# Optimization experiments

Hardware: AMD Instinct MI355X
Metric: run time of the kernel (lower is better)

## Reference

```python
import jax, jax.numpy as jnp
import numpy as np

B, N, E = 256, 4096, 65536  # graphs, nodes/graph (64*64), edges/graph


def setup_inputs() -> dict:
    key = jax.random.key(0)
    k = jax.random.split(key, 6)
    x = jax.random.normal(k[0], (B, N, 3), dtype=jnp.float32)
    src = jax.random.randint(k[1], (E,), 0, N, dtype=jnp.int32)
    dst = jax.random.randint(k[2], (E,), 0, N, dtype=jnp.int32)
    W1 = jax.random.normal(k[3], (3, 64), dtype=jnp.float32) * 0.3
    b1 = jnp.zeros((64,), dtype=jnp.float32)
    Wfc = jax.random.normal(k[4], (N * 64, 1), dtype=jnp.float32) * 0.002
    bfc = jnp.zeros((1,), dtype=jnp.float32)
    return {"x": x, "W1": W1, "b1": b1, "Wfc": Wfc, "bfc": bfc,
            "src": src, "dst": dst}


def reference(x, W1, b1, Wfc, bfc, src, dst):
    # DGL GraphConv, norm='both': h = relu(D_in^{-1/2} A D_out^{-1/2} x W + b)
    ones = jnp.ones((E,), dtype=x.dtype)
    deg_out = jax.ops.segment_sum(ones, src, num_segments=N)
    deg_in = jax.ops.segment_sum(ones, dst, num_segments=N)
    c_src = jax.lax.rsqrt(jnp.maximum(deg_out, 1.0))  # [N]
    c_dst = jax.lax.rsqrt(jnp.maximum(deg_in, 1.0))   # [N]
    # gather normalized source features, scatter-add into destinations
    msg = (x * c_src[None, :, None])[:, src]          # [B, E, 3]
    agg = jnp.zeros_like(x).at[:, dst].add(msg)       # [B, N, 3]
    h = jax.nn.relu((agg * c_dst[None, :, None]) @ W1 + b1)  # [B, N, 64]
    # fc: flatten per graph, Linear(N*64 -> 1) + sigmoid
    logits = h.reshape(x.shape[0], -1) @ Wfc + bfc    # [B, 1]
    return jax.nn.sigmoid(logits)
```

## Files before the change

kernel.cpp:

```cpp
#include <hip/hip_runtime.h>
#include <math.h>

#define Bg 256
#define Nn 4096
#define Ee 65536
#define Kk (Nn * 3)

__device__ __forceinline__ unsigned bf16r(float v) {
    unsigned b = __float_as_uint(v);
    return (b + 0x7fffu + ((b >> 16) & 1u)) >> 16;
}

__global__ __launch_bounds__(256) void k_prep(const int* __restrict__ src,
                                              const int* __restrict__ dst,
                                              int* __restrict__ deg_out,
                                              int* __restrict__ cursor,
                                              int* __restrict__ csr) {
    int e = blockIdx.x * 256 + threadIdx.x;
    if (e < Ee) {
        int s = src[e], d = dst[e];
        atomicAdd(&deg_out[s], 1);
        int ofs = atomicAdd(&cursor[d], 1) & 63;
        csr[(d << 6) + ofs] = s;
    }
}

__global__ __launch_bounds__(256) void k_transpose(const float* __restrict__ x,
                                                   const int* __restrict__ deg_out,
                                                   uint2* __restrict__ xsb) {
    __shared__ float4 tile4[64][49];
    __shared__ float cs[64];
    int t = threadIdx.x;
    int n0 = blockIdx.x * 64;
    int bq = blockIdx.y;
    if (t < 64) cs[t] = rsqrtf(fmaxf((float)deg_out[n0 + t], 1.0f));
    const float* xb = x + (size_t)bq * 64 * Kk + (size_t)n0 * 3;
#pragma unroll
    for (int i = 0; i < 12; i++) {
        int idx = i * 256 + t;
        int bi = idx / 48, j = idx - bi * 48;
        tile4[bi][j] = ((const float4*)(xb + (size_t)bi * Kk))[j];
    }
    __syncthreads();
    const float* tile = (const float*)tile4;
    uint2* outp = xsb + ((size_t)bq * Nn + n0) * 64;
#pragma unroll
    for (int i = 0; i < 16; i++) {
        int idx = i * 256 + t;
        int nn = idx >> 6, bl = idx & 63;
        float c = cs[nn];
        float f0 = tile[bl * 196 + nn * 3 + 0] * c;
        float f1 = tile[bl * 196 + nn * 3 + 1] * c;
        float f2 = tile[bl * 196 + nn * 3 + 2] * c;
        uint2 u;
        u.x = bf16r(f0) | (bf16r(f1) << 16);
        u.y = bf16r(f2);
        outp[(size_t)nn * 64 + bl] = u;
    }
}

__global__ __launch_bounds__(256) void k_main(const uint2* __restrict__ xsb,
                                              const float* __restrict__ W1,
                                              const float* __restrict__ b1,
                                              const float* __restrict__ Wfc,
                                              const int* __restrict__ cursor,
                                              const int* __restrict__ csr,
                                              float* __restrict__ partial) {
    __shared__ float4 sW14[64];
    __shared__ float sWfc[4][64];
    __shared__ float red[4][64];
    int t = threadIdx.x & 63;
    int w = threadIdx.x >> 6;
    int bq = blockIdx.x & 3;
    int g  = blockIdx.x >> 2;
    int n  = g * 4 + w;
    if (w == 0) sW14[t] = make_float4(W1[t], W1[64 + t], W1[128 + t], b1[t]);
    sWfc[w][t] = Wfc[n * 64 + t];
    __syncthreads();

    const uint2* slab = xsb + (size_t)bq * (Nn * 64);
    int myedge = csr[(n << 6) + t];
    int deg = cursor[n]; if (deg > 64) deg = 64;
    float a0 = 0.f, a1 = 0.f, a2 = 0.f;
    float c0 = 0.f, c1 = 0.f, c2 = 0.f;
    int i = 0;
    for (; i + 4 <= deg; i += 4) {
        int s0 = __shfl(myedge, i);
        int s1 = __shfl(myedge, i + 1);
        int s2 = __shfl(myedge, i + 2);
        int s3 = __shfl(myedge, i + 3);
        uint2 u0 = slab[(s0 << 6) + t];
        uint2 u1 = slab[(s1 << 6) + t];
        uint2 u2 = slab[(s2 << 6) + t];
        uint2 u3 = slab[(s3 << 6) + t];
        a0 += __uint_as_float(u0.x << 16); a1 += __uint_as_float(u0.x & 0xffff0000u); a2 += __uint_as_float(u0.y << 16);
        c0 += __uint_as_float(u1.x << 16); c1 += __uint_as_float(u1.x & 0xffff0000u); c2 += __uint_as_float(u1.y << 16);
        a0 += __uint_as_float(u2.x << 16); a1 += __uint_as_float(u2.x & 0xffff0000u); a2 += __uint_as_float(u2.y << 16);
        c0 += __uint_as_float(u3.x << 16); c1 += __uint_as_float(u3.x & 0xffff0000u); c2 += __uint_as_float(u3.y << 16);
    }
    for (; i < deg; i++) {
        int s = __shfl(myedge, i);
        uint2 u = slab[(s << 6) + t];
        a0 += __uint_as_float(u.x << 16);
        a1 += __uint_as_float(u.x & 0xffff0000u);
        a2 += __uint_as_float(u.y << 16);
    }
    a0 += c0; a1 += c1; a2 += c2;
    float cd = rsqrtf(fmaxf((float)deg, 1.0f));
    a0 *= cd; a1 *= cd; a2 *= cd;

    float part = 0.f;
#pragma unroll 8
    for (int f = 0; f < 64; f++) {
        float4 wv = sW14[f];
        float h = fmaf(a0, wv.x, fmaf(a1, wv.y, fmaf(a2, wv.z, wv.w)));
        part = fmaf(fmaxf(h, 0.f), sWfc[w][f], part);
    }
    red[w][t] = part;
    __syncthreads();
    if (w == 0) {
        float tot = (red[0][t] + red[1][t]) + (red[2][t] + red[3][t]);
        partial[(size_t)g * 256 + bq * 64 + t] = tot;
    }
}

__global__ __launch_bounds__(256) void k_reduce(const float* __restrict__ partial,
                                                float* __restrict__ out_acc) {
    int t = threadIdx.x;
    int g0 = blockIdx.x * 16;
    float s = 0.f;
#pragma unroll
    for (int g = 0; g < 16; g++) s += partial[(size_t)(g0 + g) * 256 + t];
    atomicAdd(&out_acc[t], s);
}

__global__ __launch_bounds__(256) void k_final(const float* __restrict__ out_acc,
                                               const float* __restrict__ bfc,
                                               float* __restrict__ out) {
    int t = threadIdx.x;
    float v = out_acc[t] + bfc[0];
    out[t] = 1.0f / (1.0f + expf(-v));
}

extern "C" void kernel_launch(void* const* d_in, const int* in_sizes, int n_in,
                              void* d_out, int out_size, void* d_ws, size_t ws_size,
                              hipStream_t stream) {
    const float* x   = (const float*)d_in[0];
    const float* W1  = (const float*)d_in[1];
    const float* b1  = (const float*)d_in[2];
    const float* Wfc = (const float*)d_in[3];
    const float* bfc = (const float*)d_in[4];
    const int*   src = (const int*)d_in[5];
    const int*   dst = (const int*)d_in[6];
    float* out = (float*)d_out;

    char* ws = (char*)d_ws;
    uint2* xsb = (uint2*)ws;
    const size_t Z = (size_t)4 * Nn * 64 * 8;
    int*   deg_out = (int*)(ws + Z);
    int*   cursor  = (int*)(ws + Z + 16384);
    float* out_acc = (float*)(ws + Z + 32768);
    int*   csr     = (int*)(ws + Z + 33792);
    float* partial = (float*)(ws + Z + 33792 + 1048576);

    hipMemsetAsync(ws + Z, 0, 33792, stream);
    k_prep<<<Ee / 256, 256, 0, stream>>>(src, dst, deg_out, cursor, csr);
    k_transpose<<<dim3(Nn / 64, 4), 256, 0, stream>>>(x, deg_out, xsb);
    k_main<<<1024 * 4, 256, 0, stream>>>(xsb, W1, b1, Wfc, cursor, csr, partial);
    k_reduce<<<64, 256, 0, stream>>>(partial, out_acc);
    k_final<<<1, 256, 0, stream>>>(out_acc, bfc, out);
}
```

Before: 108.6 us.

## Fuse reduce and sigmoid kernels, loop node groups in main, nontemporal transpose stores

The separate reduce and final-sigmoid kernels are merged into one. A ticket counter lets the last block apply the bias and sigmoid, which removes one launch. k_main now runs a quarter as many blocks, and each block loops over four node groups, so the W1 shared-memory setup cost is spread over more work. The transpose writes its bf16 output with 64-bit nontemporal stores, which may keep that data out of cache just before k_main reads it back.

```diff
diff --git a/kernel.cpp b/kernel.cpp
--- a/kernel.cpp
+++ b/kernel.cpp
@@ -27,7 +27,7 @@
 
 __global__ __launch_bounds__(256) void k_transpose(const float* __restrict__ x,
                                                    const int* __restrict__ deg_out,
-                                                   uint2* __restrict__ xsb) {
+                                                   unsigned long long* __restrict__ xsb) {
     __shared__ float4 tile4[64][49];
     __shared__ float cs[64];
     int t = threadIdx.x;
@@ -43,7 +43,7 @@
     }
     __syncthreads();
     const float* tile = (const float*)tile4;
-    uint2* outp = xsb + ((size_t)bq * Nn + n0) * 64;
+    unsigned long long* outp = xsb + ((size_t)bq * Nn + n0) * 64;
 #pragma unroll
     for (int i = 0; i < 16; i++) {
         int idx = i * 256 + t;
@@ -52,10 +52,9 @@
         float f0 = tile[bl * 196 + nn * 3 + 0] * c;
         float f1 = tile[bl * 196 + nn * 3 + 1] * c;
         float f2 = tile[bl * 196 + nn * 3 + 2] * c;
-        uint2 u;
-        u.x = bf16r(f0) | (bf16r(f1) << 16);
-        u.y = bf16r(f2);
-        outp[(size_t)nn * 64 + bl] = u;
+        unsigned long long u = (unsigned long long)(bf16r(f0) | (bf16r(f1) << 16))
+                             | ((unsigned long long)bf16r(f2) << 32);
+        __builtin_nontemporal_store(u, &outp[(size_t)nn * 64 + bl]);
     }
 }
 
@@ -72,74 +71,84 @@
     int t = threadIdx.x & 63;
     int w = threadIdx.x >> 6;
     int bq = blockIdx.x & 3;
-    int g  = blockIdx.x >> 2;
-    int n  = g * 4 + w;
+    int g0 = (blockIdx.x >> 2) * 4;
     if (w == 0) sW14[t] = make_float4(W1[t], W1[64 + t], W1[128 + t], b1[t]);
-    sWfc[w][t] = Wfc[n * 64 + t];
     __syncthreads();
+    const uint2* slab = xsb + (size_t)bq * (Nn * 64);
 
-    const uint2* slab = xsb + (size_t)bq * (Nn * 64);
-    int myedge = csr[(n << 6) + t];
-    int deg = cursor[n]; if (deg > 64) deg = 64;
-    float a0 = 0.f, a1 = 0.f, a2 = 0.f;
-    float c0 = 0.f, c1 = 0.f, c2 = 0.f;
-    int i = 0;
-    for (; i + 4 <= deg; i += 4) {
-        int s0 = __shfl(myedge, i);
-        int s1 = __shfl(myedge, i + 1);
-        int s2 = __shfl(myedge, i + 2);
-        int s3 = __shfl(myedge, i + 3);
-        uint2 u0 = slab[(s0 << 6) + t];
-        uint2 u1 = slab[(s1 << 6) + t];
-        uint2 u2 = slab[(s2 << 6) + t];
-        uint2 u3 = slab[(s3 << 6) + t];
-        a0 += __uint_as_float(u0.x << 16); a1 += __uint_as_float(u0.x & 0xffff0000u); a2 += __uint_as_float(u0.y << 16);
-        c0 += __uint_as_float(u1.x << 16); c1 += __uint_as_float(u1.x & 0xffff0000u); c2 += __uint_as_float(u1.y << 16);
-        a0 += __uint_as_float(u2.x << 16); a1 += __uint_as_float(u2.x & 0xffff0000u); a2 += __uint_as_float(u2.y << 16);
-        c0 += __uint_as_float(u3.x << 16); c1 += __uint_as_float(u3.x & 0xffff0000u); c2 += __uint_as_float(u3.y << 16);
-    }
-    for (; i < deg; i++) {
-        int s = __shfl(myedge, i);
-        uint2 u = slab[(s << 6) + t];
-        a0 += __uint_as_float(u.x << 16);
-        a1 += __uint_as_float(u.x & 0xffff0000u);
-        a2 += __uint_as_float(u.y << 16);
-    }
-    a0 += c0; a1 += c1; a2 += c2;
-    float cd = rsqrtf(fmaxf((float)deg, 1.0f));
-    a0 *= cd; a1 *= cd; a2 *= cd;
+    for (int gi = 0; gi < 4; gi++) {
+        int g = g0 + gi;
+        int n = g * 4 + w;
+        sWfc[w][t] = Wfc[n * 64 + t];
 
-    float part = 0.f;
+        int deg = cursor[n]; if (deg > 64) deg = 64;
+        int myedge = csr[(n << 6) + t];
+        if (t >= deg) myedge = 0;
+        float a0 = 0.f, a1 = 0.f, a2 = 0.f;
+        float c0 = 0.f, c1 = 0.f, c2 = 0.f;
+        int i = 0;
+        for (; i + 4 <= deg; i += 4) {
+            int s0 = __shfl(myedge, i);
+            int s1 = __shfl(myedge, i + 1);
+            int s2 = __shfl(myedge, i + 2);
+            int s3 = __shfl(myedge, i + 3);
+            uint2 u0 = slab[(s0 << 6) + t];
+            uint2 u1 = slab[(s1 << 6) + t];
+            uint2 u2 = slab[(s2 << 6) + t];
+            uint2 u3 = slab[(s3 << 6) + t];
+            a0 += __uint_as_float(u0.x << 16); a1 += __uint_as_float(u0.x & 0xffff0000u); a2 += __uint_as_float(u0.y << 16);
+            c0 += __uint_as_float(u1.x << 16); c1 += __uint_as_float(u1.x & 0xffff0000u); c2 += __uint_as_float(u1.y << 16);
+            a0 += __uint_as_float(u2.x << 16); a1 += __uint_as_float(u2.x & 0xffff0000u); a2 += __uint_as_float(u2.y << 16);
+            c0 += __uint_as_float(u3.x << 16); c1 += __uint_as_float(u3.x & 0xffff0000u); c2 += __uint_as_float(u3.y << 16);
+        }
+        for (; i < deg; i++) {
+            int s = __shfl(myedge, i);
+            uint2 u = slab[(s << 6) + t];
+            a0 += __uint_as_float(u.x << 16);
+            a1 += __uint_as_float(u.x & 0xffff0000u);
+            a2 += __uint_as_float(u.y << 16);
+        }
+        a0 += c0; a1 += c1; a2 += c2;
+        float cd = rsqrtf(fmaxf((float)deg, 1.0f));
+        a0 *= cd; a1 *= cd; a2 *= cd;
+
+        __syncthreads();
+        float part = 0.f;
 #pragma unroll 8
-    for (int f = 0; f < 64; f++) {
-        float4 wv = sW14[f];
-        float h = fmaf(a0, wv.x, fmaf(a1, wv.y, fmaf(a2, wv.z, wv.w)));
-        part = fmaf(fmaxf(h, 0.f), sWfc[w][f], part);
-    }
-    red[w][t] = part;
-    __syncthreads();
-    if (w == 0) {
-        float tot = (red[0][t] + red[1][t]) + (red[2][t] + red[3][t]);
-        partial[(size_t)g * 256 + bq * 64 + t] = tot;
+        for (int f = 0; f < 64; f++) {
+            float4 wv = sW14[f];
+            float h = fmaf(a0, wv.x, fmaf(a1, wv.y, fmaf(a2, wv.z, wv.w)));
+            part = fmaf(fmaxf(h, 0.f), sWfc[w][f], part);
+        }
+        red[w][t] = part;
+        __syncthreads();
+        if (w == 0) {
+            float tot = (red[0][t] + red[1][t]) + (red[2][t] + red[3][t]);
+            partial[(size_t)g * 256 + bq * 64 + t] = tot;
+        }
     }
 }
 
-__global__ __launch_bounds__(256) void k_reduce(const float* __restrict__ partial,
-                                                float* __restrict__ out_acc) {
+__global__ __launch_bounds__(256) void k_reduce_final(const float* __restrict__ partial,
+                                                      float* __restrict__ out_acc,
+                                                      int* __restrict__ ticket,
+                                                      const float* __restrict__ bfc,
+                                                      float* __restrict__ out) {
+    __shared__ int lastflag;
     int t = threadIdx.x;
     int g0 = blockIdx.x * 16;
     float s = 0.f;
 #pragma unroll
     for (int g = 0; g < 16; g++) s += partial[(size_t)(g0 + g) * 256 + t];
     atomicAdd(&out_acc[t], s);
-}
-
-__global__ __launch_bounds__(256) void k_final(const float* __restrict__ out_acc,
-                                               const float* __restrict__ bfc,
-                                               float* __restrict__ out) {
-    int t = threadIdx.x;
-    float v = out_acc[t] + bfc[0];
-    out[t] = 1.0f / (1.0f + expf(-v));
+    __threadfence();
+    __syncthreads();
+    if (t == 0) lastflag = (atomicAdd(ticket, 1) == 63);
+    __syncthreads();
+    if (lastflag) {
+        float v = atomicAdd(&out_acc[t], 0.0f) + bfc[0];
+        out[t] = 1.0f / (1.0f + expf(-v));
+    }
 }
 
 extern "C" void kernel_launch(void* const* d_in, const int* in_sizes, int n_in,
@@ -160,13 +169,13 @@
     int*   deg_out = (int*)(ws + Z);
     int*   cursor  = (int*)(ws + Z + 16384);
     float* out_acc = (float*)(ws + Z + 32768);
-    int*   csr     = (int*)(ws + Z + 33792);
-    float* partial = (float*)(ws + Z + 33792 + 1048576);
+    int*   ticket  = (int*)(ws + Z + 33792);
+    int*   csr     = (int*)(ws + Z + 33920);
+    float* partial = (float*)(ws + Z + 33920 + 1048576);
 
-    hipMemsetAsync(ws + Z, 0, 33792, stream);
+    hipMemsetAsync(ws + Z, 0, 33796, stream);
     k_prep<<<Ee / 256, 256, 0, stream>>>(src, dst, deg_out, cursor, csr);
-    k_transpose<<<dim3(Nn / 64, 4), 256, 0, stream>>>(x, deg_out, xsb);
-    k_main<<<1024 * 4, 256, 0, stream>>>(xsb, W1, b1, Wfc, cursor, csr, partial);
-    k_reduce<<<64, 256, 0, stream>>>(partial, out_acc);
-    k_final<<<1, 256, 0, stream>>>(out_acc, bfc, out);
+    k_transpose<<<dim3(Nn / 64, 4), 256, 0, stream>>>(x, deg_out, (unsigned long long*)xsb);
+    k_main<<<1024, 256, 0, stream>>>(xsb, W1, b1, Wfc, cursor, csr, partial);
+    k_reduce_final<<<64, 256, 0, stream>>>(partial, out_acc, ticket, bfc, out);
 }
```

Result: slower. 118.2 us (+8.9%).
